# Kernel optimization log

Hardware: AMD Instinct MI355X
Metric: run time of the kernel (lower is better)

The kernel has to match this reference:

```python
import jax, jax.numpy as jnp
import numpy as np

B, S, H, L, C = 32, 512, 768, 512, 3  # batch, seq, hidden, max_length, num_classes


def _lin_init(k, fan_in, shape):
    return jax.random.normal(k, shape, jnp.float32) * (1.0 / np.sqrt(fan_in))


def setup_inputs() -> dict:
    key = jax.random.key(0)
    ks = jax.random.split(key, 18)
    return {
        "tokens": jax.random.normal(ks[0], (B, S, H), jnp.float32),
        # shared Q/K/V projections (used for both token- and feature-attention)
        "Wq": _lin_init(ks[1], H, (H, H)), "bq": jnp.zeros((H,), jnp.float32),
        "Wk": _lin_init(ks[2], H, (H, H)), "bk": jnp.zeros((H,), jnp.float32),
        "Wv": _lin_init(ks[3], H, (H, H)), "bv": jnp.zeros((H,), jnp.float32),
        # TSGSA: Linear(H,1)+ReLU gate over tokens
        "W_ts": _lin_init(ks[4], H, (H, 1)), "b_ts": jnp.zeros((1,), jnp.float32),
        # FSGSA: Linear(max_length,1)+ReLU gate over padded seq axis (also reused for FGSA per source bug)
        "W_fs": _lin_init(ks[5], L, (L, 1)), "b_fs": jnp.zeros((1,), jnp.float32),
        # TGSA: Linear(H,H)+Sigmoid gate
        "W_tg": _lin_init(ks[6], H, (H, H)), "b_tg": jnp.zeros((H,), jnp.float32),
        # fnn: Linear(7H,H) -> Linear(H,C)
        "W1": _lin_init(ks[7], 7 * H, (7 * H, H)), "b1": jnp.zeros((H,), jnp.float32),
        "W2": _lin_init(ks[8], H, (H, C)), "b2": jnp.zeros((C,), jnp.float32),
    }


def _ln(x):
    # LayerNorm over (seq, hidden) jointly, eps=1e-8; freshly-instantiated affine params are identity
    m = jnp.mean(x, axis=(1, 2), keepdims=True)
    v = jnp.var(x, axis=(1, 2), keepdims=True)
    return (x - m) * jax.lax.rsqrt(v + 1e-8)


def reference(tokens, Wq, bq, Wk, bk, Wv, bv, W_ts, b_ts, W_fs, b_fs, W_tg, b_tg, W1, b1, W2, b2):
    scale = 1.0 / np.sqrt(H)
    Q = tokens @ Wq + bq  # [B,S,H]
    K = tokens @ Wk + bk
    V = tokens @ Wv + bv
    # token-direction self-attention: softmax(Q K^T / sqrt(H)) V
    att = jax.nn.softmax(jnp.einsum('bsh,bth->bst', Q, K) * scale, axis=-1)  # [B,S,S]
    TSA = jnp.einsum('bst,bth->bsh', att, V)
    # feature-direction self-attention: V @ softmax(Q^T K / sqrt(H))
    attN = jax.nn.softmax(jnp.einsum('bsh,bsg->bhg', Q, K) * scale, axis=-1)  # [B,H,H]
    FSA = jnp.einsum('bsh,bhg->bsg', V, attN)
    # gate branches
    TSGSA = jax.nn.relu(tokens @ W_ts + b_ts) * tokens  # [B,S,1]*[B,S,H]
    tpad = jnp.pad(tokens.transpose(0, 2, 1), ((0, 0), (0, 0), (0, L - S)))  # [B,H,L]
    gate_f = jax.nn.relu(tpad @ W_fs + b_fs)  # [B,H,1]
    FSGSA = (gate_f * tokens.transpose(0, 2, 1)).transpose(0, 2, 1)  # [B,S,H]
    TGSA = jax.nn.sigmoid(tokens @ W_tg + b_tg) * tokens
    FGSA = FSGSA  # source bug: FGSA branch applies self.FSGSA, identical to FSGSA
    out_all = jnp.concatenate(
        [tokens, _ln(TSA), _ln(FSA), _ln(TGSA), _ln(FGSA), _ln(TSGSA), _ln(FSGSA)], axis=2)  # [B,S,7H]
    pooled = jnp.mean(out_all, axis=1)  # [B,7H]
    return (pooled @ W1 + b1) @ W2 + b2  # [B,C]
```

## Files before the change

### kernel.cpp

```cpp
#include <hip/hip_runtime.h>
#include <cmath>

typedef unsigned short u16;
typedef __attribute__((ext_vector_type(4))) float f32x4;
typedef __attribute__((ext_vector_type(4))) unsigned int u32x4;
typedef __attribute__((ext_vector_type(8))) __bf16 bf16x8;

__device__ __forceinline__ u16 f2b(float f) {
  unsigned int u = __builtin_bit_cast(unsigned int, f);
  return (u16)((u + 0x7fffu + ((u >> 16) & 1u)) >> 16);
}
__device__ __forceinline__ float b2f(u16 h) {
  unsigned int u = ((unsigned int)h) << 16;
  return __builtin_bit_cast(float, u);
}

__device__ __forceinline__ void glds16(const u16* g, u16* l) {
  __builtin_amdgcn_global_load_lds(
      (const __attribute__((address_space(1))) void*)g,
      (__attribute__((address_space(3))) void*)l, 16, 0, 0);
}

template <int EPI>
__global__ __launch_bounds__(512) void gemm_f_k(
    const u16* __restrict__ Ap, const u16* __restrict__ Bp, u16* __restrict__ Cp,
    u16* __restrict__ CpT, const float* __restrict__ bias,
    const u16* __restrict__ tokp, float* __restrict__ colsum,
    float* __restrict__ bstat, int K, int lda, int ldb, int ldc, long sA,
    long sB, long sC, float scale) {
  __shared__ alignas(16) u16 Asm[2][8192];
  __shared__ alignas(16) u16 Bsm[2][4096];
  __shared__ float scol_s[128];
  __shared__ float sred[2];

  const int gx = gridDim.x, gxy = gx * gridDim.y;
  const int nwg = gxy * gridDim.z;
  int orig = (blockIdx.z * gridDim.y + blockIdx.y) * gx + blockIdx.x;
  int gwi = (orig & 7) * (nwg >> 3) + (orig >> 3);
  const int z = gwi / gxy;
  int rem = gwi - z * gxy;
  const int ty = rem / gx, tx = rem - ty * gx;
  const int tileM = ty << 8, tileN = tx << 7;

  const u16* Abase = Ap + (size_t)z * sA;
  const u16* Bbase = Bp + (size_t)z * sB;

  const int tid = threadIdx.x;
  const int lane = tid & 63, w = tid >> 6;
  const int wr = (w >> 1) << 6, wc = (w & 1) << 6;
  const int fr = lane & 15, fg = lane >> 4;

  f32x4 acc[4][4];
#pragma unroll
  for (int i = 0; i < 4; ++i)
#pragma unroll
    for (int j = 0; j < 4; ++j) acc[i][j] = (f32x4){0.f, 0.f, 0.f, 0.f};

  const int sArow = (w << 5) + (lane >> 2);
  const int sBrow = (w << 4) + (lane >> 2);
  const int scol = (((lane & 3) ^ ((lane >> 3) & 3)) << 3);
  const u16* gA = Abase + (size_t)(tileM + sArow) * lda + scol;
  const u16* gB = Bbase + (size_t)(tileN + sBrow) * ldb + scol;
  const int ldsA = (w << 5) * 32;
  const int ldsB = (w << 4) * 32;

  auto STAGE = [&](int buf, int k0) {
    glds16(gA + k0, &Asm[buf][ldsA]);
    glds16(gA + (size_t)16 * lda + k0, &Asm[buf][ldsA + 512]);
    glds16(gB + k0, &Bsm[buf][ldsB]);
  };

  const int col_off = ((fg ^ ((fr >> 1) & 3)) << 3);

  const int nt = K >> 5;
  STAGE(0, 0);
  int cur = 0;
  for (int t = 0; t < nt; ++t) {
    if (t + 1 < nt) {
      STAGE(cur ^ 1, (t + 1) << 5);
      asm volatile("s_waitcnt vmcnt(3)" ::: "memory");
    } else {
      asm volatile("s_waitcnt vmcnt(0)" ::: "memory");
    }
    __builtin_amdgcn_s_barrier();
    asm volatile("" ::: "memory");
    const u16* Ab = Asm[cur];
    const u16* Bb = Bsm[cur];
    bf16x8 av[4], bw[4];
#pragma unroll
    for (int m = 0; m < 4; ++m)
      av[m] = *(const bf16x8*)&Ab[(wr + (m << 4) + fr) * 32 + col_off];
#pragma unroll
    for (int n = 0; n < 4; ++n)
      bw[n] = *(const bf16x8*)&Bb[(wc + (n << 4) + fr) * 32 + col_off];
#pragma unroll
    for (int m = 0; m < 4; ++m)
#pragma unroll
      for (int n = 0; n < 4; ++n)
        acc[m][n] =
            __builtin_amdgcn_mfma_f32_16x16x32_bf16(av[m], bw[n], acc[m][n], 0, 0, 0);
    asm volatile("" ::: "memory");
    __builtin_amdgcn_s_barrier();
    cur ^= 1;
  }

  if constexpr (EPI == 0) {
    const int cbuf = tileN / 768;
    const int nbase = tileN - cbuf * 768;
    u16* Cz = Cp + (size_t)cbuf * sC;
#pragma unroll
    for (int m = 0; m < 4; ++m) {
#pragma unroll
      for (int n = 0; n < 4; ++n) {
        const int gcol = tileN + wc + (n << 4) + fr;
        const int lcol = nbase + wc + (n << 4) + fr;
        const float bv2 = bias[gcol];
#pragma unroll
        for (int r = 0; r < 4; ++r) {
          const int grow = tileM + wr + (m << 4) + (fg << 2) + r;
          Cz[(size_t)grow * 768 + lcol] = f2b(acc[m][n][r] + bv2);
        }
      }
    }
    u16* Ct = CpT + (size_t)cbuf * sC;
#pragma unroll
    for (int m = 0; m < 4; ++m) {
#pragma unroll
      for (int n = 0; n < 4; ++n) {
        const int gcol = tileN + wc + (n << 4) + fr;
        const int lcol = nbase + wc + (n << 4) + fr;
        const int grow0 = tileM + wr + (m << 4) + (fg << 2);
        union { u16 u[4]; unsigned long long q; } pk;
#pragma unroll
        for (int r = 0; r < 4; ++r) pk.u[r] = f2b(acc[m][n][r] + bias[gcol]);
        *(unsigned long long*)&Ct[(size_t)lcol * 16384 + grow0] = pk.q;
      }
    }
  } else if constexpr (EPI == 1) {
    if (tid < 128) scol_s[tid] = 0.f;
    if (tid == 0) { sred[0] = 0.f; sred[1] = 0.f; }
    __syncthreads();
    float ls = 0.f, lq = 0.f;
#pragma unroll
    for (int n = 0; n < 4; ++n) {
      float cpart = 0.f;
      const int gcol = tileN + wc + (n << 4) + fr;
      const float bv2 = bias[gcol];
#pragma unroll
      for (int m = 0; m < 4; ++m) {
#pragma unroll
        for (int r = 0; r < 4; ++r) {
          const int grow = tileM + wr + (m << 4) + (fg << 2) + r;
          float g = 1.f / (1.f + __expf(-(acc[m][n][r] + bv2)));
          float v = g * b2f(tokp[(size_t)grow * 768 + gcol]);
          cpart += v; ls += v; lq += v * v;
        }
      }
      atomicAdd(&scol_s[wc + (n << 4) + fr], cpart);
    }
    atomicAdd(&sred[0], ls);
    atomicAdd(&sred[1], lq);
    __syncthreads();
    const int b = tileM >> 9;
    if (tid < 128) atomicAdd(&colsum[(size_t)b * 768 + tileN + tid], scol_s[tid]);
    if (tid == 0) {
      atomicAdd(&bstat[b], sred[0]);
      atomicAdd(&bstat[32 + b], sred[1]);
    }
  } else if constexpr (EPI == 2) {
    u16* Cz = Cp + (size_t)z * sC;
#pragma unroll
    for (int m = 0; m < 4; ++m) {
#pragma unroll
      for (int n = 0; n < 4; ++n) {
        const int gcol = tileN + wc + (n << 4) + fr;
#pragma unroll
        for (int r = 0; r < 4; ++r) {
          const int grow = tileM + wr + (m << 4) + (fg << 2) + r;
          Cz[(size_t)grow * ldc + gcol] = f2b(acc[m][n][r] * scale);
        }
      }
    }
  } else {
    if (tid < 128) scol_s[tid] = 0.f;
    if (tid == 0) { sred[0] = 0.f; sred[1] = 0.f; }
    __syncthreads();
    float ls = 0.f, lq = 0.f;
#pragma unroll
    for (int n = 0; n < 4; ++n) {
      float cpart = 0.f;
#pragma unroll
      for (int m = 0; m < 4; ++m) {
#pragma unroll
        for (int r = 0; r < 4; ++r) {
          float v = acc[m][n][r];
          cpart += v; ls += v; lq += v * v;
        }
      }
      atomicAdd(&scol_s[wc + (n << 4) + fr], cpart);
    }
    atomicAdd(&sred[0], ls);
    atomicAdd(&sred[1], lq);
    __syncthreads();
    if (tid < 128) atomicAdd(&colsum[(size_t)z * 768 + tileN + tid], scol_s[tid]);
    if (tid == 0) {
      atomicAdd(&bstat[z], sred[0]);
      atomicAdd(&bstat[32 + z], sred[1]);
    }
  }
}

__global__ __launch_bounds__(256) void cvt_row_k(
    const float* __restrict__ tok, u16* __restrict__ tokb,
    const float* __restrict__ Wts, const float* __restrict__ bts,
    float* __restrict__ gate_t, float* __restrict__ rowsum,
    float* __restrict__ rowsumsq) {
  const int w = threadIdx.x >> 6, lane = threadIdx.x & 63;
  const int row = blockIdx.x * 4 + w;
  const float* p = tok + (size_t)row * 768;
  u16* q = tokb + (size_t)row * 768;
  float s = 0.f, sq = 0.f, g = 0.f;
#pragma unroll
  for (int i = 0; i < 3; ++i) {
    const int idx = (i * 64 + lane) << 2;
    f32x4 v = *(const f32x4*)(p + idx);
    f32x4 wv = *(const f32x4*)(Wts + idx);
    union { u16 u[4]; unsigned long long q8; } pk;
#pragma unroll
    for (int j = 0; j < 4; ++j) {
      s += v[j]; sq += v[j] * v[j]; g += v[j] * wv[j];
      pk.u[j] = f2b(v[j]);
    }
    *(unsigned long long*)(q + idx) = pk.q8;
  }
#pragma unroll
  for (int o = 32; o > 0; o >>= 1) {
    s += __shfl_xor(s, o); sq += __shfl_xor(sq, o); g += __shfl_xor(g, o);
  }
  if (lane == 0) {
    gate_t[row] = fmaxf(g + bts[0], 0.f);
    rowsum[row] = s;
    rowsumsq[row] = sq;
  }
}

__global__ __launch_bounds__(256) void transpose_w_k(const float* __restrict__ W,
                                                     u16* __restrict__ WT) {
  __shared__ float t[64][65];
  const int r0 = blockIdx.y << 6, c0 = blockIdx.x << 6;
  for (int i = threadIdx.x; i < 4096; i += 256) {
    int r = i >> 6, c = i & 63;
    t[r][c] = W[(size_t)(r0 + r) * 768 + c0 + c];
  }
  __syncthreads();
  for (int i = threadIdx.x; i < 4096; i += 256) {
    int rr = i >> 6, cc = i & 63;
    WT[(size_t)(c0 + rr) * 768 + r0 + cc] = f2b(t[cc][rr]);
  }
}

template <int LEN>
__global__ __launch_bounds__(256) void softmax_k(u16* __restrict__ data) {
  constexpr int NP = LEN / 256;
  const int row = blockIdx.x, tid = threadIdx.x;
  u16* p = data + (size_t)row * LEN;
  const int lane = tid & 63, wid = tid >> 6;
  float v[NP];
  float mx = -1e30f;
#pragma unroll
  for (int i = 0; i < NP; ++i) { v[i] = b2f(p[tid + (i << 8)]); mx = fmaxf(mx, v[i]); }
#pragma unroll
  for (int o = 32; o > 0; o >>= 1) mx = fmaxf(mx, __shfl_xor(mx, o));
  __shared__ float red[4], red2[4];
  if (lane == 0) red[wid] = mx;
  __syncthreads();
  mx = fmaxf(fmaxf(red[0], red[1]), fmaxf(red[2], red[3]));
  float sum = 0.f;
#pragma unroll
  for (int i = 0; i < NP; ++i) { v[i] = __expf(v[i] - mx); sum += v[i]; }
#pragma unroll
  for (int o = 32; o > 0; o >>= 1) sum += __shfl_xor(sum, o);
  if (lane == 0) red2[wid] = sum;
  __syncthreads();
  sum = red2[0] + red2[1] + red2[2] + red2[3];
  const float inv = 1.f / sum;
#pragma unroll
  for (int i = 0; i < NP; ++i) p[tid + (i << 8)] = f2b(v[i] * inv);
}

__global__ __launch_bounds__(256) void colsoftmax_k(u16* __restrict__ data) {
  __shared__ u16 tile[32][72];
  __shared__ float sm[4][64], ss[4][64];
  const int tid = threadIdx.x;
  const int b = blockIdx.x;
  u16* base = data + (size_t)b * 589824 + (blockIdx.y << 6);
  const int lr = tid >> 3, seg = (tid & 7) << 3;
  const int c = tid & 63, q = tid >> 6;
  float m = -1e30f, s = 0.f;
  for (int ch = 0; ch < 24; ++ch) {
    u16* g = base + (size_t)(ch * 32 + lr) * 768 + seg;
    *(u32x4*)&tile[lr][seg] = *(const u32x4*)g;
    __syncthreads();
#pragma unroll
    for (int i = 0; i < 8; ++i) {
      float v = b2f(tile[(q << 3) + i][c]);
      float mn = fmaxf(m, v);
      s = s * __expf(m - mn) + __expf(v - mn);
      m = mn;
    }
    __syncthreads();
  }
  sm[q][c] = m; ss[q][c] = s;
  __syncthreads();
  const float M = fmaxf(fmaxf(sm[0][c], sm[1][c]), fmaxf(sm[2][c], sm[3][c]));
  const float S = ss[0][c] * __expf(sm[0][c] - M) + ss[1][c] * __expf(sm[1][c] - M) +
                  ss[2][c] * __expf(sm[2][c] - M) + ss[3][c] * __expf(sm[3][c] - M);
  const float inv = 1.f / S;
  for (int ch = 0; ch < 24; ++ch) {
    u16* g = base + (size_t)(ch * 32 + lr) * 768 + seg;
    *(u32x4*)&tile[lr][seg] = *(const u32x4*)g;
    __syncthreads();
#pragma unroll
    for (int i = 0; i < 8; ++i) {
      const int r = (q << 3) + i;
      tile[r][c] = f2b(__expf(b2f(tile[r][c]) - M) * inv);
    }
    __syncthreads();
    *(u32x4*)g = *(const u32x4*)&tile[lr][seg];
    __syncthreads();
  }
}

__global__ __launch_bounds__(256) void col_stats_k(
    const u16* __restrict__ tokb, const float* __restrict__ Wfs,
    const float* __restrict__ bfs, const float* __restrict__ gate_t,
    float* __restrict__ gate_f, float* __restrict__ colsum_tok,
    float* __restrict__ colsumsq_tok, float* __restrict__ colsum_tsg) {
  const int b = blockIdx.x, h = blockIdx.y * 256 + threadIdx.x;
  const u16* p = tokb + (size_t)b * 512 * 768 + h;
  const float* gt = gate_t + b * 512;
  float cs = 0.f, cq = 0.f, gf = 0.f, tg = 0.f;
#pragma unroll 4
  for (int s = 0; s < 512; ++s) {
    float t = b2f(p[(size_t)s * 768]);
    cs += t; cq += t * t; gf += t * Wfs[s]; tg += t * gt[s];
  }
  const int idx = b * 768 + h;
  gate_f[idx] = fmaxf(gf + bfs[0], 0.f);
  colsum_tok[idx] = cs;
  colsumsq_tok[idx] = cq;
  colsum_tsg[idx] = tg;
}

__global__ __launch_bounds__(256) void batch_stats_k(
    const float* __restrict__ gate_t, const float* __restrict__ rowsum,
    const float* __restrict__ rowsumsq, const float* __restrict__ gate_f,
    const float* __restrict__ colsum_tok, const float* __restrict__ colsumsq_tok,
    float* __restrict__ st) {
  __shared__ float red[4][256];
  const int b = blockIdx.x, tid = threadIdx.x;
  float ts = 0.f, tq = 0.f, fs = 0.f, fq = 0.f;
  for (int s = tid; s < 512; s += 256) {
    float g = gate_t[b * 512 + s];
    ts += g * rowsum[b * 512 + s];
    tq += g * g * rowsumsq[b * 512 + s];
  }
  for (int h = tid; h < 768; h += 256) {
    float g = gate_f[b * 768 + h];
    fs += g * colsum_tok[b * 768 + h];
    fq += g * g * colsumsq_tok[b * 768 + h];
  }
  red[0][tid] = ts; red[1][tid] = tq; red[2][tid] = fs; red[3][tid] = fq;
  __syncthreads();
  for (int o = 128; o > 0; o >>= 1) {
    if (tid < o) {
      red[0][tid] += red[0][tid + o];
      red[1][tid] += red[1][tid + o];
      red[2][tid] += red[2][tid + o];
      red[3][tid] += red[3][tid + o];
    }
    __syncthreads();
  }
  if (tid == 0) {
    st[b] = red[0][0]; st[32 + b] = red[1][0];
    st[64 + b] = red[2][0]; st[96 + b] = red[3][0];
  }
}

__global__ __launch_bounds__(768) void pooled_k(
    const float* __restrict__ colsum_tok, const float* __restrict__ colsum_tsa,
    const float* __restrict__ bstat_tsa, const float* __restrict__ colsum_fsa,
    const float* __restrict__ bstat_fsa, const float* __restrict__ colsum_tgsa,
    const float* __restrict__ bstat_tgsa, const float* __restrict__ colsum_tsg,
    const float* __restrict__ gate_f, const float* __restrict__ st,
    float* __restrict__ pooled) {
  const int b = blockIdx.x, h = threadIdx.x;
  const float invS = 1.f / 512.f, invN = 1.f / (512.f * 768.f);
  const int i = b * 768 + h;
  float* pr = pooled + (size_t)b * 5376;
  pr[h] = colsum_tok[i] * invS;
  auto lnslot = [&](int slot, float cs, float bs, float bq) {
    float m = bs * invN;
    float var = bq * invN - m * m;
    pr[slot * 768 + h] = (cs * invS - m) * rsqrtf(var + 1e-8f);
  };
  lnslot(1, colsum_tsa[i], bstat_tsa[b], bstat_tsa[32 + b]);
  lnslot(2, colsum_fsa[i], bstat_fsa[b], bstat_fsa[32 + b]);
  lnslot(3, colsum_tgsa[i], bstat_tgsa[b], bstat_tgsa[32 + b]);
  const float fsg_cs = gate_f[i] * colsum_tok[i];
  lnslot(4, fsg_cs, st[64 + b], st[96 + b]);
  lnslot(5, colsum_tsg[i], st[b], st[32 + b]);
  lnslot(6, fsg_cs, st[64 + b], st[96 + b]);
}

__global__ __launch_bounds__(256) void fnn1_k(const float* __restrict__ pooled,
                                              const float* __restrict__ W1,
                                              float* __restrict__ tmp1) {
  __shared__ float sp[128][36];
  const int c0 = blockIdx.x << 7, k0 = blockIdx.y << 7;
  const int tid = threadIdx.x;
  for (int i = tid; i < 4096; i += 256) {
    int b = i >> 7, j = i & 127;
    sp[j][b] = pooled[(size_t)b * 5376 + k0 + j];
  }
  __syncthreads();
  const int c = c0 + (tid & 127);
  const int u = (tid >> 7) << 4;
  float acc[16];
#pragma unroll
  for (int t = 0; t < 16; ++t) acc[t] = 0.f;
#pragma unroll 4
  for (int j = 0; j < 128; ++j) {
    float w = W1[(size_t)(k0 + j) * 768 + c];
    const f32x4* row = (const f32x4*)&sp[j][u];
#pragma unroll
    for (int t4 = 0; t4 < 4; ++t4) {
      f32x4 v = row[t4];
#pragma unroll
      for (int r = 0; r < 4; ++r) acc[t4 * 4 + r] += v[r] * w;
    }
  }
#pragma unroll
  for (int t = 0; t < 16; ++t) atomicAdd(&tmp1[(u + t) * 768 + c], acc[t]);
}

__global__ __launch_bounds__(256) void fnn2_k(const float* __restrict__ tmp1,
                                              const float* __restrict__ b1,
                                              const float* __restrict__ W2,
                                              const float* __restrict__ b2,
                                              float* __restrict__ out) {
  const int gw = blockIdx.x * 4 + (threadIdx.x >> 6);
  const int lane = threadIdx.x & 63;
  const int b = gw / 3, c = gw % 3;
  float a = 0.f;
#pragma unroll
  for (int i = 0; i < 12; ++i) {
    int k = lane + i * 64;
    a += (tmp1[b * 768 + k] + b1[k]) * W2[k * 3 + c];
  }
#pragma unroll
  for (int o = 32; o > 0; o >>= 1) a += __shfl_xor(a, o);
  if (lane == 0) out[b * 3 + c] = a + b2[c];
}

extern "C" void kernel_launch(void* const* d_in, const int* in_sizes, int n_in,
                              void* d_out, int out_size, void* d_ws, size_t ws_size,
                              hipStream_t stream) {
  const float* tokens = (const float*)d_in[0];
  const float* Wq = (const float*)d_in[1];
  const float* bq = (const float*)d_in[2];
  const float* Wk = (const float*)d_in[3];
  const float* bk = (const float*)d_in[4];
  const float* Wv = (const float*)d_in[5];
  const float* bv = (const float*)d_in[6];
  const float* Wts = (const float*)d_in[7];
  const float* bts = (const float*)d_in[8];
  const float* Wfs = (const float*)d_in[9];
  const float* bfs = (const float*)d_in[10];
  const float* Wtg = (const float*)d_in[11];
  const float* btg = (const float*)d_in[12];
  const float* W1 = (const float*)d_in[13];
  const float* b1 = (const float*)d_in[14];
  const float* W2 = (const float*)d_in[15];
  const float* b2 = (const float*)d_in[16];
  float* out = (float*)d_out;

  char* ws = (char*)d_ws;
  size_t off = 0;
  auto take = [&](size_t bytes) -> char* {
    char* p = ws + off;
    off += (bytes + 255) & ~(size_t)255;
    return p;
  };
  u16* tokb = (u16*)take((size_t)16384 * 768 * 2);
  u16* WqT = (u16*)take((size_t)768 * 768 * 2);
  u16* WkT = (u16*)take((size_t)768 * 768 * 2);
  u16* WvT = (u16*)take((size_t)768 * 768 * 2);
  u16* WtgT = (u16*)take((size_t)768 * 768 * 2);
  u16* Qb = (u16*)take((size_t)16384 * 768 * 2);
  u16* Kb = (u16*)take((size_t)16384 * 768 * 2);
  u16* Vb = (u16*)take((size_t)16384 * 768 * 2);
  u16* Qt = (u16*)take((size_t)768 * 16384 * 2);
  u16* Kt = (u16*)take((size_t)768 * 16384 * 2);
  u16* Vt = (u16*)take((size_t)768 * 16384 * 2);
  u16* attb = (u16*)take((size_t)32 * 512 * 512 * 2);
  u16* attNt = (u16*)take((size_t)32 * 768 * 768 * 2);
  float* bias3 = (float*)take(2304 * 4);
  char* zbase = ws + off;
  float* colsum_tsa = (float*)take(24576 * 4);
  float* colsum_fsa = (float*)take(24576 * 4);
  float* colsum_tgsa = (float*)take(24576 * 4);
  float* bstat_tsa = (float*)take(64 * 4);
  float* bstat_fsa = (float*)take(64 * 4);
  float* bstat_tgsa = (float*)take(64 * 4);
  float* tmp1 = (float*)take((size_t)32 * 768 * 4);
  size_t zbytes = (size_t)((ws + off) - zbase);
  float* colsum_tsg = (float*)take(24576 * 4);
  float* gate_t = (float*)take(16384 * 4);
  float* rowsum = (float*)take(16384 * 4);
  float* rowsumsq = (float*)take(16384 * 4);
  float* gate_f = (float*)take(24576 * 4);
  float* colsum_tok = (float*)take(24576 * 4);
  float* colsumsq_tok = (float*)take(24576 * 4);
  float* st4 = (float*)take(128 * 4);
  float* pooled = (float*)take((size_t)32 * 5376 * 4);

  hipMemsetAsync(zbase, 0, zbytes, stream);
  hipMemcpyAsync(bias3, bq, 768 * 4, hipMemcpyDeviceToDevice, stream);
  hipMemcpyAsync(bias3 + 768, bk, 768 * 4, hipMemcpyDeviceToDevice, stream);
  hipMemcpyAsync(bias3 + 1536, bv, 768 * 4, hipMemcpyDeviceToDevice, stream);

  const float scale = 1.0f / sqrtf(768.0f);
  const dim3 blk(256);
  const dim3 blk512(512);

  cvt_row_k<<<4096, blk, 0, stream>>>(tokens, tokb, Wts, bts, gate_t, rowsum,
                                      rowsumsq);
  transpose_w_k<<<dim3(12, 12), blk, 0, stream>>>(Wq, WqT);
  transpose_w_k<<<dim3(12, 12), blk, 0, stream>>>(Wk, WkT);
  transpose_w_k<<<dim3(12, 12), blk, 0, stream>>>(Wv, WvT);
  transpose_w_k<<<dim3(12, 12), blk, 0, stream>>>(Wtg, WtgT);

  gemm_f_k<0><<<dim3(18, 64, 1), blk512, 0, stream>>>(
      tokb, WqT, Qb, Qt, bias3, nullptr, nullptr, nullptr, 768, 768, 768, 768,
      0, 0, 12582912, 0.f);
  gemm_f_k<1><<<dim3(6, 64, 1), blk512, 0, stream>>>(
      tokb, WtgT, nullptr, nullptr, btg, tokb, colsum_tgsa, bstat_tgsa, 768,
      768, 768, 0, 0, 0, 0, 0.f);

  gemm_f_k<2><<<dim3(6, 3, 32), blk512, 0, stream>>>(
      Kt, Qt, attNt, nullptr, nullptr, nullptr, nullptr, nullptr, 512, 16384,
      16384, 768, 512, 512, 589824, scale);
  colsoftmax_k<<<dim3(32, 12), blk, 0, stream>>>(attNt);

  gemm_f_k<2><<<dim3(4, 2, 32), blk512, 0, stream>>>(
      Qb, Kb, attb, nullptr, nullptr, nullptr, nullptr, nullptr, 768, 768, 768,
      512, 393216, 393216, 262144, scale);
  softmax_k<512><<<16384, 256, 0, stream>>>(attb);

  gemm_f_k<3><<<dim3(6, 2, 32), blk512, 0, stream>>>(
      attb, Vt, nullptr, nullptr, nullptr, nullptr, colsum_tsa, bstat_tsa, 512,
      512, 16384, 0, 262144, 512, 0, 0.f);
  gemm_f_k<3><<<dim3(6, 2, 32), blk512, 0, stream>>>(
      Vb, attNt, nullptr, nullptr, nullptr, nullptr, colsum_fsa, bstat_fsa, 768,
      768, 768, 0, 393216, 589824, 0, 0.f);

  col_stats_k<<<dim3(32, 3), blk, 0, stream>>>(tokb, Wfs, bfs, gate_t, gate_f,
                                               colsum_tok, colsumsq_tok, colsum_tsg);
  batch_stats_k<<<32, blk, 0, stream>>>(gate_t, rowsum, rowsumsq, gate_f,
                                        colsum_tok, colsumsq_tok, st4);

  pooled_k<<<32, 768, 0, stream>>>(colsum_tok, colsum_tsa, bstat_tsa, colsum_fsa,
                                   bstat_fsa, colsum_tgsa, bstat_tgsa, colsum_tsg,
                                   gate_f, st4, pooled);
  fnn1_k<<<dim3(6, 42), blk, 0, stream>>>(pooled, W1, tmp1);
  fnn2_k<<<24, blk, 0, stream>>>(tmp1, b1, W2, b2, out);
}
```

Baseline: 438.2 us.

## Fuse column softmax max/sum stats into feature-attention GEMM epilogue, per-batch transposed layout

The feature-attention GEMM epilogue now computes per-tile column maxima and exp-sums and writes them as partials. The separate column-softmax kernel then only merges three partials per column and normalizes, so it no longer makes a first full read pass over the 768x768 attention matrices. The transposed Q/K/V buffers are also laid out per batch ([32][768][512] rather than [768][16384]), which shortens the strides seen by the consuming GEMMs. The epilogue gains extra shared-memory reductions and syncs, and it recomputes exps of the accumulators.

```diff
diff --git a/kernel.cpp b/kernel.cpp
--- a/kernel.cpp
+++ b/kernel.cpp
@@ -123,17 +123,19 @@
       }
     }
     u16* Ct = CpT + (size_t)cbuf * sC;
+    const int zb = tileM >> 9;
+    const int sbase = tileM & 511;
 #pragma unroll
     for (int m = 0; m < 4; ++m) {
 #pragma unroll
       for (int n = 0; n < 4; ++n) {
         const int gcol = tileN + wc + (n << 4) + fr;
         const int lcol = nbase + wc + (n << 4) + fr;
-        const int grow0 = tileM + wr + (m << 4) + (fg << 2);
+        const int srow0 = sbase + wr + (m << 4) + (fg << 2);
         union { u16 u[4]; unsigned long long q; } pk;
 #pragma unroll
         for (int r = 0; r < 4; ++r) pk.u[r] = f2b(acc[m][n][r] + bias[gcol]);
-        *(unsigned long long*)&Ct[(size_t)lcol * 16384 + grow0] = pk.q;
+        *(unsigned long long*)&Ct[((size_t)(zb * 768 + lcol) << 9) + srow0] = pk.q;
       }
     }
   } else if constexpr (EPI == 1) {
@@ -180,6 +182,64 @@
           Cz[(size_t)grow * ldc + gcol] = f2b(acc[m][n][r] * scale);
         }
       }
+    }
+  } else if constexpr (EPI == 4) {
+    u16* Cz = Cp + (size_t)z * sC;
+    float lmax[4];
+#pragma unroll
+    for (int n = 0; n < 4; ++n) {
+      const int gcol = tileN + wc + (n << 4) + fr;
+      float mx = -1e30f;
+#pragma unroll
+      for (int m = 0; m < 4; ++m) {
+#pragma unroll
+        for (int r = 0; r < 4; ++r) {
+          const int grow = tileM + wr + (m << 4) + (fg << 2) + r;
+          float v = acc[m][n][r] * scale;
+          Cz[(size_t)grow * ldc + gcol] = f2b(v);
+          mx = fmaxf(mx, v);
+        }
+      }
+      lmax[n] = mx;
+    }
+    float* red = (float*)&Asm[0][0];
+    const int slot = ((w >> 1) << 2) + fg;
+    __syncthreads();
+#pragma unroll
+    for (int n = 0; n < 4; ++n)
+      red[slot * 132 + wc + (n << 4) + fr] = lmax[n];
+    __syncthreads();
+    if (tid < 128) {
+      float m2 = red[tid];
+#pragma unroll
+      for (int i = 1; i < 16; ++i) m2 = fmaxf(m2, red[i * 132 + tid]);
+      scol_s[tid] = m2;
+    }
+    __syncthreads();
+    float lsum[4];
+#pragma unroll
+    for (int n = 0; n < 4; ++n) {
+      const float M = scol_s[wc + (n << 4) + fr];
+      float s2 = 0.f;
+#pragma unroll
+      for (int m = 0; m < 4; ++m)
+#pragma unroll
+        for (int r = 0; r < 4; ++r) s2 += __expf(acc[m][n][r] * scale - M);
+      lsum[n] = s2;
+    }
+    __syncthreads();
+#pragma unroll
+    for (int n = 0; n < 4; ++n)
+      red[slot * 132 + wc + (n << 4) + fr] = lsum[n];
+    __syncthreads();
+    if (tid < 128) {
+      float s2 = 0.f;
+#pragma unroll
+      for (int i = 0; i < 16; ++i) s2 += red[i * 132 + tid];
+      const int ty3 = tileM >> 8;
+      const size_t pidx = ((size_t)z * 3 + ty3) * 768 + tileN + tid;
+      colsum[pidx] = scol_s[tid];
+      bstat[pidx] = s2;
     }
   } else {
     if (tid < 128) scol_s[tid] = 0.f;
@@ -288,33 +348,20 @@
   for (int i = 0; i < NP; ++i) p[tid + (i << 8)] = f2b(v[i] * inv);
 }
 
-__global__ __launch_bounds__(256) void colsoftmax_k(u16* __restrict__ data) {
+__global__ __launch_bounds__(256) void colnorm_k(u16* __restrict__ data,
+                                                 const float* __restrict__ pmax,
+                                                 const float* __restrict__ psum) {
   __shared__ u16 tile[32][72];
-  __shared__ float sm[4][64], ss[4][64];
   const int tid = threadIdx.x;
   const int b = blockIdx.x;
   u16* base = data + (size_t)b * 589824 + (blockIdx.y << 6);
   const int lr = tid >> 3, seg = (tid & 7) << 3;
   const int c = tid & 63, q = tid >> 6;
-  float m = -1e30f, s = 0.f;
-  for (int ch = 0; ch < 24; ++ch) {
-    u16* g = base + (size_t)(ch * 32 + lr) * 768 + seg;
-    *(u32x4*)&tile[lr][seg] = *(const u32x4*)g;
-    __syncthreads();
-#pragma unroll
-    for (int i = 0; i < 8; ++i) {
-      float v = b2f(tile[(q << 3) + i][c]);
-      float mn = fmaxf(m, v);
-      s = s * __expf(m - mn) + __expf(v - mn);
-      m = mn;
-    }
-    __syncthreads();
-  }
-  sm[q][c] = m; ss[q][c] = s;
-  __syncthreads();
-  const float M = fmaxf(fmaxf(sm[0][c], sm[1][c]), fmaxf(sm[2][c], sm[3][c]));
-  const float S = ss[0][c] * __expf(sm[0][c] - M) + ss[1][c] * __expf(sm[1][c] - M) +
-                  ss[2][c] * __expf(sm[2][c] - M) + ss[3][c] * __expf(sm[3][c] - M);
+  const size_t p0 = (size_t)b * 3 * 768 + (blockIdx.y << 6) + c;
+  const float m0 = pmax[p0], m1 = pmax[p0 + 768], m2 = pmax[p0 + 1536];
+  const float M = fmaxf(fmaxf(m0, m1), m2);
+  const float S = psum[p0] * __expf(m0 - M) + psum[p0 + 768] * __expf(m1 - M) +
+                  psum[p0 + 1536] * __expf(m2 - M);
   const float inv = 1.f / S;
   for (int ch = 0; ch < 24; ++ch) {
     u16* g = base + (size_t)(ch * 32 + lr) * 768 + seg;
@@ -500,12 +547,14 @@
   u16* Qb = (u16*)take((size_t)16384 * 768 * 2);
   u16* Kb = (u16*)take((size_t)16384 * 768 * 2);
   u16* Vb = (u16*)take((size_t)16384 * 768 * 2);
-  u16* Qt = (u16*)take((size_t)768 * 16384 * 2);
-  u16* Kt = (u16*)take((size_t)768 * 16384 * 2);
-  u16* Vt = (u16*)take((size_t)768 * 16384 * 2);
+  u16* Qt = (u16*)take((size_t)32 * 768 * 512 * 2);
+  u16* Kt = (u16*)take((size_t)32 * 768 * 512 * 2);
+  u16* Vt = (u16*)take((size_t)32 * 768 * 512 * 2);
   u16* attb = (u16*)take((size_t)32 * 512 * 512 * 2);
   u16* attNt = (u16*)take((size_t)32 * 768 * 768 * 2);
   float* bias3 = (float*)take(2304 * 4);
+  float* pmax = (float*)take((size_t)32 * 3 * 768 * 4);
+  float* psum = (float*)take((size_t)32 * 3 * 768 * 4);
   char* zbase = ws + off;
   float* colsum_tsa = (float*)take(24576 * 4);
   float* colsum_fsa = (float*)take(24576 * 4);
@@ -548,10 +597,10 @@
       tokb, WtgT, nullptr, nullptr, btg, tokb, colsum_tgsa, bstat_tgsa, 768,
       768, 768, 0, 0, 0, 0, 0.f);
 
-  gemm_f_k<2><<<dim3(6, 3, 32), blk512, 0, stream>>>(
-      Kt, Qt, attNt, nullptr, nullptr, nullptr, nullptr, nullptr, 512, 16384,
-      16384, 768, 512, 512, 589824, scale);
-  colsoftmax_k<<<dim3(32, 12), blk, 0, stream>>>(attNt);
+  gemm_f_k<4><<<dim3(6, 3, 32), blk512, 0, stream>>>(
+      Kt, Qt, attNt, nullptr, nullptr, nullptr, pmax, psum, 512, 512, 512, 768,
+      393216, 393216, 589824, scale);
+  colnorm_k<<<dim3(32, 12), blk, 0, stream>>>(attNt, pmax, psum);
 
   gemm_f_k<2><<<dim3(4, 2, 32), blk512, 0, stream>>>(
       Qb, Kb, attb, nullptr, nullptr, nullptr, nullptr, nullptr, 768, 768, 768,
@@ -560,7 +609,7 @@
 
   gemm_f_k<3><<<dim3(6, 2, 32), blk512, 0, stream>>>(
       attb, Vt, nullptr, nullptr, nullptr, nullptr, colsum_tsa, bstat_tsa, 512,
-      512, 16384, 0, 262144, 512, 0, 0.f);
+      512, 512, 0, 262144, 393216, 0, 0.f);
   gemm_f_k<3><<<dim3(6, 2, 32), blk512, 0, stream>>>(
       Vb, attNt, nullptr, nullptr, nullptr, nullptr, colsum_fsa, bstat_fsa, 768,
       768, 768, 0, 393216, 589824, 0, 0.f);
```

Result: faster. 418.8 us (-4.4%).
